# Performance work log

Hardware: AMD Instinct MI355X
Metric: run time of the kernel (lower is better)

Reference implementation:

```python
import jax, jax.numpy as jnp
import numpy as np

D_MODEL = 1024


def setup_inputs() -> dict:
    key = jax.random.key(0)
    ks = jax.random.split(key, 7)
    s = 1.0 / np.sqrt(D_MODEL)
    return {
        "x": jax.random.normal(ks[0], (4, 4096, D_MODEL), dtype=jnp.float32),
        "Wq": jax.random.normal(ks[1], (D_MODEL, D_MODEL), dtype=jnp.float32) * s,
        "bq": jax.random.normal(ks[2], (D_MODEL,), dtype=jnp.float32) * s,
        "Wk": jax.random.normal(ks[3], (D_MODEL, D_MODEL), dtype=jnp.float32) * s,
        "bk": jax.random.normal(ks[4], (D_MODEL,), dtype=jnp.float32) * s,
        "Wv": jax.random.normal(ks[5], (D_MODEL, D_MODEL), dtype=jnp.float32) * s,
        "bv": jax.random.normal(ks[6], (D_MODEL,), dtype=jnp.float32) * s,
    }


def reference(x, Wq, bq, Wk, bk, Wv, bv):
    # nn.Linear: y = x @ W.T + b
    Q = jnp.einsum("bsd,ed->bse", x, Wq) + bq  # [B,S,D]
    K = jnp.einsum("bsd,ed->bse", x, Wk) + bk
    V = jnp.einsum("bsd,ed->bse", x, Wv) + bv
    scale = 1.0 / jnp.sqrt(jnp.asarray(x.shape[-1], dtype=x.dtype))
    KV = jnp.einsum("bsd,bse->bde", K, V) * scale  # [B,D,D]
    E = jnp.einsum("bsd,bde->bse", Q, KV)  # [B,S,D]
    return E
```

## Files before the change

### kernel.cpp

```cpp
#include <hip/hip_runtime.h>
#include <hip/hip_fp16.h>


#define BATCH 4
#define SEQ   4096
#define DM    1024

typedef _Float16 h8 __attribute__((ext_vector_type(8)));
typedef _Float16 h4 __attribute__((ext_vector_type(4)));
typedef float    f4 __attribute__((ext_vector_type(4)));

__device__ inline void gload_lds16(const _Float16* g, _Float16* l) {
    __builtin_amdgcn_global_load_lds(
        (const __attribute__((address_space(1))) void*)g,
        (__attribute__((address_space(3))) void*)l,
        16, 0, 0);
}

__device__ inline int xcd_swz(int bid, int grid) {
    const int q = grid >> 3;
    return (bid & 7) * q + (bid >> 3);
}

__device__ inline float doth(const _Float16* wr, const float* v, int lane) {
    float s = 0.f;
    #pragma unroll
    for (int i = 0; i < 2; ++i) {
        const int k = i * 512 + lane * 8;
        h8 wv = *(const h8*)&wr[k];
        f4 v0 = *(const f4*)&v[k];
        f4 v1 = *(const f4*)&v[k + 4];
        s += (float)wv[0] * v0.x + (float)wv[1] * v0.y +
             (float)wv[2] * v0.z + (float)wv[3] * v0.w +
             (float)wv[4] * v1.x + (float)wv[5] * v1.y +
             (float)wv[6] * v1.z + (float)wv[7] * v1.w;
    }
    return s;
}
__device__ inline float dotf(const float* a, const float* b, int lane) {
    float s = 0.f;
    #pragma unroll
    for (int i = 0; i < 4; ++i) {
        const int k = i * 256 + lane * 4;
        f4 x = *(const f4*)&a[k];
        f4 y = *(const f4*)&b[k];
        s += x.x * y.x + x.y * y.y + x.z * y.z + x.w * y.w;
    }
    return s;
}
__device__ inline float wred(float s) {
    #pragma unroll
    for (int off = 32; off; off >>= 1) s += __shfl_down(s, off);
    return s;
}

__global__ __launch_bounds__(256) void cvt_x(
    const float* __restrict__ src, _Float16* __restrict__ dstT,
    _Float16* __restrict__ dstRM, int R, int C)
{
    __shared__ float tile[64][65];
    const long zoff = (long)blockIdx.z * R * C;
    src += zoff; dstT += zoff; dstRM += zoff;
    const int r0 = blockIdx.y * 64;
    const int c0 = blockIdx.x * 64;
    const int t  = threadIdx.x;
    const int tr = t >> 4;
    const int tc = (t & 15) * 4;
    #pragma unroll
    for (int i = 0; i < 4; ++i) {
        const int r = tr + i * 16;
        f4 v = *(const f4*)&src[(long)(r0 + r) * C + c0 + tc];
        tile[r][tc + 0] = v.x; tile[r][tc + 1] = v.y;
        tile[r][tc + 2] = v.z; tile[r][tc + 3] = v.w;
        h4 h = { (_Float16)v.x, (_Float16)v.y, (_Float16)v.z, (_Float16)v.w };
        *(h4*)&dstRM[(long)(r0 + r) * C + c0 + tc] = h;
    }
    __syncthreads();
    #pragma unroll
    for (int i = 0; i < 4; ++i) {
        const int c = tr + i * 16;
        h4 h = { (_Float16)tile[tc + 0][c], (_Float16)tile[tc + 1][c],
                 (_Float16)tile[tc + 2][c], (_Float16)tile[tc + 3][c] };
        *(h4*)&dstT[(long)(c0 + c) * R + r0 + tc] = h;
    }
}

__global__ __launch_bounds__(256) void wcvt(
    const float* __restrict__ Wq, const float* __restrict__ Wk,
    const float* __restrict__ Wv,
    _Float16* __restrict__ Wqt, _Float16* __restrict__ Wkt,
    _Float16* __restrict__ Wkh, _Float16* __restrict__ Wvh)
{
    __shared__ float tile[64][65];
    const int z = blockIdx.z;
    const float* src = z == 0 ? Wq : (z == 1 ? Wk : Wv);
    _Float16* dstT  = z == 0 ? Wqt : (z == 1 ? Wkt : nullptr);
    _Float16* dstRM = z == 0 ? nullptr : (z == 1 ? Wkh : Wvh);
    const int r0 = blockIdx.y * 64;
    const int c0 = blockIdx.x * 64;
    const int t  = threadIdx.x;
    const int tr = t >> 4;
    const int tc = (t & 15) * 4;
    #pragma unroll
    for (int i = 0; i < 4; ++i) {
        const int r = tr + i * 16;
        f4 v = *(const f4*)&src[(long)(r0 + r) * DM + c0 + tc];
        tile[r][tc + 0] = v.x; tile[r][tc + 1] = v.y;
        tile[r][tc + 2] = v.z; tile[r][tc + 3] = v.w;
        if (dstRM) {
            h4 h = { (_Float16)v.x, (_Float16)v.y, (_Float16)v.z, (_Float16)v.w };
            *(h4*)&dstRM[(long)(r0 + r) * DM + c0 + tc] = h;
        }
    }
    __syncthreads();
    if (dstT) {
        #pragma unroll
        for (int i = 0; i < 4; ++i) {
            const int c = tr + i * 16;
            h4 h = { (_Float16)tile[tc + 0][c], (_Float16)tile[tc + 1][c],
                     (_Float16)tile[tc + 2][c], (_Float16)tile[tc + 3][c] };
            *(h4*)&dstT[(long)(c0 + c) * DM + r0 + tc] = h;
        }
    }
}

__global__ __launch_bounds__(256) void rowsum_xt(
    const _Float16* __restrict__ xt, float* __restrict__ xs)
{
    const int gw   = blockIdx.x * 4 + (threadIdx.x >> 6);
    const int lane = threadIdx.x & 63;
    const _Float16* row = xt + (long)gw * SEQ;
    float s = 0.f;
    #pragma unroll
    for (int i = 0; i < SEQ; i += 512) {
        h8 v = *(const h8*)&row[i + lane * 8];
        #pragma unroll
        for (int j = 0; j < 8; ++j) s += (float)v[j];
    }
    s = wred(s);
    if (lane == 0) xs[gw] = s;
}

__global__ __launch_bounds__(256) void gemv_misc(
    const _Float16* __restrict__ Wvh, const _Float16* __restrict__ Wkh,
    const _Float16* __restrict__ Wqt, const _Float16* __restrict__ Wkt,
    const float* __restrict__ xs, const float* __restrict__ bv,
    const float* __restrict__ bk, const float* __restrict__ bq,
    float* __restrict__ vecs)
{
    const int gw   = blockIdx.x * 4 + (threadIdx.x >> 6);
    const int lane = threadIdx.x & 63;
    const _Float16* wr;
    const float* v;
    if (gw < 4096)      { wr = Wvh + (long)(gw & 1023) * DM; v = xs + (gw >> 10) * DM; }
    else if (gw < 8192) { wr = Wkh + (long)(gw & 1023) * DM; v = xs + ((gw - 4096) >> 10) * DM; }
    else if (gw < 9216) { wr = Wqt + (long)(gw - 8192) * DM; v = bk; }
    else                { wr = Wkt + (long)(gw - 9216) * DM; v = bq; }
    float s = wred(doth(wr, v, lane));
    if (lane == 0) {
        if (gw < 4096) s += (float)SEQ * bv[gw & 1023];
        vecs[gw] = s;
    }
}

__global__ __launch_bounds__(256) void gemv_qw(
    const _Float16* __restrict__ Wqt, const float* __restrict__ w,
    const float* __restrict__ bq, const float* __restrict__ bk,
    float* __restrict__ qw, float* __restrict__ sv)
{
    const int gw   = blockIdx.x * 4 + (threadIdx.x >> 6);
    const int lane = threadIdx.x & 63;
    if (gw < 4096) {
        float s = wred(doth(Wqt + (long)(gw & 1023) * DM, w + (gw >> 10) * DM, lane));
        if (lane == 0) qw[gw] = s;
    } else if (gw == 4096) {
        float s = wred(dotf(bq, bk, lane));
        if (lane == 0) sv[0] = s;
    } else if (gw <= 4100) {
        float s = wred(dotf(bq, w + (gw - 4097) * DM, lane));
        if (lane == 0) sv[1 + (gw - 4097)] = s;
    }
}

__global__ __launch_bounds__(256) void gemv_cv(
    const _Float16* __restrict__ Ph, const float* __restrict__ kb,
    const float* __restrict__ u2, const float* __restrict__ bv,
    const float* __restrict__ sv, float* __restrict__ cv)
{
    const int gw   = blockIdx.x * 4 + (threadIdx.x >> 6);
    const int lane = threadIdx.x & 63;
    const int b    = gw >> 10;
    const int e    = gw & 1023;
    float s = wred(doth(Ph + (long)b * DM * DM + (long)e * DM, kb, lane));
    if (lane == 0)
        cv[gw] = s + (sv[0] * u2[gw] + sv[1 + b] * bv[e]) * 0.03125f;
}

__global__ __launch_bounds__(256) void reduce_gh(
    const _Float16* __restrict__ parts, _Float16* __restrict__ Gh)
{
    const long DD_ = (long)DM * DM;
    const long i = ((long)blockIdx.x * 256 + threadIdx.x) * 8;
    const long b = i >> 20;
    const long r = i & (DD_ - 1);
    const _Float16* p = parts + b * 4 * DD_ + r;
    h8 v0 = *(const h8*)&p[0];
    h8 v1 = *(const h8*)&p[DD_];
    h8 v2 = *(const h8*)&p[2 * DD_];
    h8 v3 = *(const h8*)&p[3 * DD_];
    h8 o;
    #pragma unroll
    for (int j = 0; j < 8; ++j) {
        float s = (float)v0[j] + (float)v1[j] + (float)v2[j] + (float)v3[j];
        o[j] = (_Float16)(s * 0.03125f);
    }
    *(h8*)&Gh[i] = o;
}

template<typename OutT, int BIAS>
__global__ __launch_bounds__(512, 1) void gemm8p(
    const _Float16* __restrict__ A, const _Float16* __restrict__ B,
    OutT* __restrict__ C,
    int K, int lda, int ldb, int ldc, int tilesX, int perZ,
    long aZ, long bZ, long cZ, int sk, long aK, long bK,
    const float* __restrict__ bc1, long bc1Z, float alpha)
{
    __shared__ _Float16 lds[2 * 32768];

    const int L  = xcd_swz(blockIdx.x, gridDim.x);
    const int z  = L / perZ;
    const int r0 = L - z * perZ;
    const int zb = z / sk;
    const int zk = z - zb * sk;
    A += (long)zb * aZ + (long)zk * aK;
    B += (long)zb * bZ + (long)zk * bK;
    C += (long)z * cZ;
    const float* pc1 = (BIAS == 1) ? bc1 + (long)zb * bc1Z : nullptr;

    const int tileM = (r0 / tilesX) * 256;
    const int tileN = (r0 % tilesX) * 256;
    const int tid   = threadIdx.x;
    const int lane  = tid & 63;
    const int wave  = tid >> 6;
    const int wr    = wave >> 2;
    const int wc    = wave & 3;
    const int la    = lane & 15;
    const int kg    = lane >> 4;

    auto stageA = [&](int buf, int mq, int kt) {
        _Float16* dst = &lds[buf * 32768 + mq * 8192];
        const int k0 = kt * 64;
        #pragma unroll
        for (int i = 0; i < 2; ++i) {
            const int U = i * 512 + tid;
            const int R = U >> 3, s = U & 7;
            const int gr = tileM + (R >> 6) * 128 + mq * 64 + (R & 63);
            gload_lds16(&A[(long)gr * lda + k0 + ((s ^ (R & 7)) << 3)], dst + U * 8);
        }
    };
    auto stageB = [&](int buf, int nq, int kt) {
        _Float16* dst = &lds[buf * 32768 + 16384 + nq * 8192];
        const int k0 = kt * 64;
        #pragma unroll
        for (int i = 0; i < 2; ++i) {
            const int U = i * 512 + tid;
            const int R = U >> 3, s = U & 7;
            const int gn = tileN + (R >> 5) * 64 + nq * 32 + (R & 31);
            gload_lds16(&B[(long)gn * ldb + k0 + ((s ^ (R & 7)) << 3)], dst + U * 8);
        }
    };

    f4 acc[8][4] = {};
    h8 af[4][2];
    h8 bf[2][2][2];

    auto readA = [&](int buf, int mq) {
        const _Float16* Ab = &lds[buf * 32768 + mq * 8192];
        #pragma unroll
        for (int mi = 0; mi < 4; ++mi)
            #pragma unroll
            for (int kk = 0; kk < 2; ++kk) {
                const int R = wr * 64 + mi * 16 + la;
                const int s = kk * 4 + kg;
                af[mi][kk] = *(const h8*)&Ab[R * 64 + ((s ^ (R & 7)) << 3)];
            }
    };
    auto readB = [&](int buf, int nq) {
        const _Float16* Bb = &lds[buf * 32768 + 16384 + nq * 8192];
        #pragma unroll
        for (int ni = 0; ni < 2; ++ni)
            #pragma unroll
            for (int kk = 0; kk < 2; ++kk) {
                const int R = wc * 32 + ni * 16 + la;
                const int s = kk * 4 + kg;
                bf[nq][ni][kk] = *(const h8*)&Bb[R * 64 + ((s ^ (R & 7)) << 3)];
            }
    };
    auto mfmaQ = [&](int mq, int nq) {
        __builtin_amdgcn_s_setprio(1);
        #pragma unroll
        for (int mi = 0; mi < 4; ++mi)
            #pragma unroll
            for (int ni = 0; ni < 2; ++ni)
                #pragma unroll
                for (int kk = 0; kk < 2; ++kk)
                    acc[mq * 4 + mi][nq * 2 + ni] =
                        __builtin_amdgcn_mfma_f32_16x16x32_f16(
                            af[mi][kk], bf[nq][ni][kk],
                            acc[mq * 4 + mi][nq * 2 + ni], 0, 0, 0);
        __builtin_amdgcn_s_setprio(0);
    };

    const int NT = K >> 6;

    stageA(0, 0, 0); stageA(0, 1, 0); stageB(0, 0, 0); stageB(0, 1, 0);
    if (NT > 1) {
        stageA(1, 0, 1); stageB(1, 0, 1);
        asm volatile("s_waitcnt vmcnt(4)" ::: "memory");
    } else {
        asm volatile("s_waitcnt vmcnt(0)" ::: "memory");
    }
    __builtin_amdgcn_sched_barrier(0);
    __builtin_amdgcn_s_barrier();

    for (int j = 0; j < NT; ++j) {
        const int buf = j & 1;
        readA(buf, 0); readB(buf, 0);
        if (j + 1 < NT) stageA(buf ^ 1, 1, j + 1);
        asm volatile("s_waitcnt lgkmcnt(8)" ::: "memory");
        __builtin_amdgcn_s_barrier();
        asm volatile("s_waitcnt lgkmcnt(0)" ::: "memory");
        __builtin_amdgcn_sched_barrier(0);
        mfmaQ(0, 0);
        __builtin_amdgcn_s_barrier();
        readB(buf, 1);
        if (j + 1 < NT) stageB(buf ^ 1, 1, j + 1);
        __builtin_amdgcn_s_barrier();
        asm volatile("s_waitcnt lgkmcnt(0)" ::: "memory");
        __builtin_amdgcn_sched_barrier(0);
        mfmaQ(0, 1);
        __builtin_amdgcn_s_barrier();
        readA(buf, 1);
        if (j + 2 < NT) stageA(buf, 0, j + 2);
        __builtin_amdgcn_s_barrier();
        asm volatile("s_waitcnt lgkmcnt(0)" ::: "memory");
        __builtin_amdgcn_sched_barrier(0);
        mfmaQ(1, 0);
        __builtin_amdgcn_s_barrier();
        if (j + 2 < NT) stageB(buf, 0, j + 2);
        __builtin_amdgcn_s_barrier();
        mfmaQ(1, 1);
        if (j + 2 < NT) {
            asm volatile("s_waitcnt vmcnt(4)" ::: "memory");
        } else if (j + 1 < NT) {
            asm volatile("s_waitcnt vmcnt(0)" ::: "memory");
        }
        __builtin_amdgcn_sched_barrier(0);
        __builtin_amdgcn_s_barrier();
    }

    #pragma unroll
    for (int mf = 0; mf < 8; ++mf) {
        #pragma unroll
        for (int nf = 0; nf < 4; ++nf) {
            const int col = tileN + wc * 64 + nf * 16 + la;
            #pragma unroll
            for (int jj = 0; jj < 4; ++jj) {
                const int row = tileM + wr * 128 + mf * 16 + kg * 4 + jj;
                float v = acc[mf][nf][jj] * alpha;
                if (BIAS == 1) v += pc1[col];
                C[(long)row * ldc + col] = (OutT)v;
            }
        }
    }
}

template<int BIAS>
__global__ __launch_bounds__(256) void gemm64(
    const _Float16* __restrict__ A, const _Float16* __restrict__ B,
    _Float16* __restrict__ C,
    const _Float16* __restrict__ A2, const _Float16* __restrict__ B2,
    _Float16* __restrict__ C2, int zSplit,
    int K, int lda, int ldb, int ldc, int tilesX, int perZ,
    long aZ, long bZ, long cZ,
    const float* __restrict__ bc1, long bc1Z,
    const float* __restrict__ br1, long br1Z,
    const float* __restrict__ bc2, long bc2Z,
    const float* __restrict__ br2, long br2Z,
    float alpha, float beta)
{
    __shared__ _Float16 As[64 * 64];
    __shared__ _Float16 Bs[64 * 64];

    const int L  = xcd_swz(blockIdx.x, gridDim.x);
    int z        = L / perZ;
    const int r0 = L - z * perZ;
    if (z >= zSplit) { A = A2; B = B2; C = C2; z = 0; }
    A += (long)z * aZ;
    B += (long)z * bZ;
    C += (long)z * cZ;
    const float* pc1 = nullptr; const float* pr1 = nullptr;
    const float* pc2 = nullptr; const float* pr2 = nullptr;
    if (BIAS == 3) {
        pc1 = bc1 + (long)z * bc1Z; pr1 = br1 + (long)z * br1Z;
        pc2 = bc2 + (long)z * bc2Z; pr2 = br2 + (long)z * br2Z;
    }

    const int tileM = (r0 / tilesX) * 64;
    const int tileN = (r0 % tilesX) * 64;
    const int tid   = threadIdx.x;
    const int lane  = tid & 63;
    const int wave  = tid >> 6;
    const int wm    = (wave >> 1) * 32;
    const int wn    = (wave & 1) * 32;
    const int srow  = tid >> 3;
    const int sslot = tid & 7;

    f4 acc[2][2] = {};
    const int arow = lane & 15;
    const int kg   = lane >> 4;

    for (int k0 = 0; k0 < K; k0 += 64) {
        #pragma unroll
        for (int i = 0; i < 2; ++i) {
            const int row   = i * 32 + srow;
            const int gslot = sslot ^ (row & 7);
            gload_lds16(&A[(long)(tileM + row) * lda + k0 + gslot * 8],
                        &As[row * 64 + sslot * 8]);
            gload_lds16(&B[(long)(tileN + row) * ldb + k0 + gslot * 8],
                        &Bs[row * 64 + sslot * 8]);
        }
        __syncthreads();

        #pragma unroll
        for (int kk = 0; kk < 64; kk += 32) {
            h8 af[2], bf[2];
            #pragma unroll
            for (int m = 0; m < 2; ++m) {
                const int rr   = wm + m * 16 + arow;
                const int slot = (kk >> 3) + kg;
                af[m] = *(const h8*)&As[rr * 64 + ((slot ^ (rr & 7)) << 3)];
            }
            #pragma unroll
            for (int n = 0; n < 2; ++n) {
                const int rr   = wn + n * 16 + arow;
                const int slot = (kk >> 3) + kg;
                bf[n] = *(const h8*)&Bs[rr * 64 + ((slot ^ (rr & 7)) << 3)];
            }
            #pragma unroll
            for (int m = 0; m < 2; ++m)
                #pragma unroll
                for (int n = 0; n < 2; ++n)
                    acc[m][n] = __builtin_amdgcn_mfma_f32_16x16x32_f16(
                        af[m], bf[n], acc[m][n], 0, 0, 0);
        }
        __syncthreads();
    }

    #pragma unroll
    for (int m = 0; m < 2; ++m) {
        #pragma unroll
        for (int n = 0; n < 2; ++n) {
            const int col = tileN + wn + n * 16 + arow;
            #pragma unroll
            for (int j = 0; j < 4; ++j) {
                const int row = tileM + wm + m * 16 + (lane >> 4) * 4 + j;
                float v = acc[m][n][j] * alpha;
                if (BIAS == 3) v += beta * (pc1[col] * pr1[row] + pc2[col] * pr2[row]);
                C[(long)row * ldc + col] = (_Float16)v;
            }
        }
    }
}

extern "C" void kernel_launch(void* const* d_in, const int* in_sizes, int n_in,
                              void* d_out, int out_size, void* d_ws, size_t ws_size,
                              hipStream_t stream)
{
    const float* x  = (const float*)d_in[0];
    const float* Wq = (const float*)d_in[1];
    const float* bq = (const float*)d_in[2];
    const float* Wk = (const float*)d_in[3];
    const float* bk = (const float*)d_in[4];
    const float* Wv = (const float*)d_in[5];
    const float* bv = (const float*)d_in[6];
    float* out = (float*)d_out;

    const long DD = (long)DM * DM;
    const long DS = (long)DM * SEQ;
    const long MB = 1024l * 1024;

    char* base = (char*)d_ws;
    _Float16* xh   = (_Float16*)base;
    _Float16* xt   = (_Float16*)(base + 32 * MB);
    _Float16* Gh   = xt;
    _Float16* Ph   = (_Float16*)(base + 40 * MB);
    _Float16* Rth  = (_Float16*)(base + 48 * MB);
    _Float16* Wqt  = (_Float16*)(base + 64 * MB);
    _Float16* Wkh  = (_Float16*)(base + 66 * MB);
    _Float16* Wvh  = (_Float16*)(base + 68 * MB);
    _Float16* Wkt  = (_Float16*)(base + 70 * MB);
    _Float16* Mh   = (_Float16*)(base + 72 * MB);
    float*    vecs = (float*)(base + 74 * MB);
    float*    u2   = vecs;
    float*    w    = vecs + 4096;
    float*    qk   = vecs + 8192;
    float*    kb   = vecs + 9216;
    float*    xs   = vecs + 10240;
    float*    qw   = vecs + 14336;
    float*    cv   = vecs + 18432;
    float*    sv   = vecs + 22528;
    _Float16* parts = (_Float16*)d_out;

    cvt_x<<<dim3(16, 64, 4), 256, 0, stream>>>(x, xt, xh, SEQ, DM);
    wcvt<<<dim3(16, 16, 3), 256, 0, stream>>>(Wq, Wk, Wv, Wqt, Wkt, Wkh, Wvh);

    rowsum_xt<<<1024, 256, 0, stream>>>(xt, xs);

    gemv_misc<<<2560, 256, 0, stream>>>(Wvh, Wkh, Wqt, Wkt, xs, bv, bk, bq, vecs);

    gemv_qw<<<1026, 256, 0, stream>>>(Wqt, w, bq, bk, qw, sv);

    gemm8p<_Float16, 0><<<256, 512, 0, stream>>>(
        xt, xt, parts, 1024, SEQ, SEQ, DM, 4, 16,
        DS, DS, DD, 4, 1024, 1024, nullptr, 0, 1.0f);

    reduce_gh<<<2048, 256, 0, stream>>>(parts, Gh);

    gemm64<0><<<1280, 256, 0, stream>>>(
        Wvh, Gh, Ph, Wqt, Wkt, Mh, 4,
        1024, DM, DM, DM, 16, 256,
        0, DD, DD,
        nullptr, 0, nullptr, 0, nullptr, 0, nullptr, 0, 1.0f, 0.f);

    gemv_cv<<<1024, 256, 0, stream>>>(Ph, kb, u2, bv, sv, cv);

    gemm64<3><<<1024, 256, 0, stream>>>(
        Ph, Mh, Rth, nullptr, nullptr, nullptr, 99,
        1024, DM, DM, DM, 16, 256,
        DD, 0, DD,
        qk, 0, u2, 1024, qw, 1024, bv, 0, 1.0f, 0.03125f);

    gemm8p<float, 1><<<256, 512, 0, stream>>>(
        xh, Rth, out, 1024, DM, DM, DM, 4, 64,
        DS, DD, DS, 1, 0, 0, cv, 1024, 1.0f);
}
```

Baseline: 168.1 us.

## Exploit symmetry of Gram matrix with triangular split-K tiles and fuse rowsum

The x^T x Gram product is now computed only for the 10 upper-triangular 256x256 tiles per batch. Each tile is split into 6 K-chunks of uneven length so 240 blocks cover the work, and a new reduce kernel sums the partials and mirrors off-diagonal tiles via an LDS transpose. The separate column-sum kernel is removed; cvt_x now accumulates the sums with atomicAdd after a memset. This cuts redundant MFMA work and one kernel launch, at the cost of fp32 atomics and a more complex reduce.

```diff
diff --git a/kernel.cpp b/kernel.cpp
--- a/kernel.cpp
+++ b/kernel.cpp
@@ -56,9 +56,10 @@
 
 __global__ __launch_bounds__(256) void cvt_x(
     const float* __restrict__ src, _Float16* __restrict__ dstT,
-    _Float16* __restrict__ dstRM, int R, int C)
+    _Float16* __restrict__ dstRM, float* __restrict__ xs, int R, int C)
 {
     __shared__ float tile[64][65];
+    __shared__ float red[4][64];
     const long zoff = (long)blockIdx.z * R * C;
     src += zoff; dstT += zoff; dstRM += zoff;
     const int r0 = blockIdx.y * 64;
@@ -83,6 +84,18 @@
                  (_Float16)tile[tc + 2][c], (_Float16)tile[tc + 3][c] };
         *(h4*)&dstT[(long)(c0 + c) * R + r0 + tc] = h;
     }
+    {
+        const int cc = t & 63;
+        const int rb = (t >> 6) * 16;
+        float ps = 0.f;
+        #pragma unroll
+        for (int r = 0; r < 16; ++r) ps += tile[rb + r][cc];
+        red[t >> 6][cc] = ps;
+    }
+    __syncthreads();
+    if (t < 64)
+        atomicAdd(&xs[blockIdx.z * DM + c0 + t],
+                  red[0][t] + red[1][t] + red[2][t] + red[3][t]);
 }
 
 __global__ __launch_bounds__(256) void wcvt(
@@ -122,23 +135,6 @@
             *(h4*)&dstT[(long)(c0 + c) * DM + r0 + tc] = h;
         }
     }
-}
-
-__global__ __launch_bounds__(256) void rowsum_xt(
-    const _Float16* __restrict__ xt, float* __restrict__ xs)
-{
-    const int gw   = blockIdx.x * 4 + (threadIdx.x >> 6);
-    const int lane = threadIdx.x & 63;
-    const _Float16* row = xt + (long)gw * SEQ;
-    float s = 0.f;
-    #pragma unroll
-    for (int i = 0; i < SEQ; i += 512) {
-        h8 v = *(const h8*)&row[i + lane * 8];
-        #pragma unroll
-        for (int j = 0; j < 8; ++j) s += (float)v[j];
-    }
-    s = wred(s);
-    if (lane == 0) xs[gw] = s;
 }
 
 __global__ __launch_bounds__(256) void gemv_misc(
@@ -196,28 +192,54 @@
         cv[gw] = s + (sv[0] * u2[gw] + sv[1 + b] * bv[e]) * 0.03125f;
 }
 
-__global__ __launch_bounds__(256) void reduce_gh(
+__global__ __launch_bounds__(256) void reduce_tri(
     const _Float16* __restrict__ parts, _Float16* __restrict__ Gh)
 {
+    __shared__ _Float16 lds[64][72];
+    const int bid = blockIdx.x;
+    const int job = bid >> 4;
+    const int ch  = bid & 15;
+    const int b   = job / 10;
+    const int p   = job - b * 10;
+    const int ti  = p >= 6 ? 3 : (p >= 3 ? 2 : (p >= 1 ? 1 : 0));
+    const int tj  = p - ((ti * (ti + 1)) >> 1);
+    const int li  = (ch >> 2) * 64;
+    const int lj  = (ch & 3) * 64;
+    const int t   = threadIdx.x;
+    const int c8  = (t & 7) * 8;
     const long DD_ = (long)DM * DM;
-    const long i = ((long)blockIdx.x * 256 + threadIdx.x) * 8;
-    const long b = i >> 20;
-    const long r = i & (DD_ - 1);
-    const _Float16* p = parts + b * 4 * DD_ + r;
-    h8 v0 = *(const h8*)&p[0];
-    h8 v1 = *(const h8*)&p[DD_];
-    h8 v2 = *(const h8*)&p[2 * DD_];
-    h8 v3 = *(const h8*)&p[3 * DD_];
-    h8 o;
-    #pragma unroll
-    for (int j = 0; j < 8; ++j) {
-        float s = (float)v0[j] + (float)v1[j] + (float)v2[j] + (float)v3[j];
-        o[j] = (_Float16)(s * 0.03125f);
-    }
-    *(h8*)&Gh[i] = o;
-}
-
-template<typename OutT, int BIAS>
+
+    h8 o[2];
+    #pragma unroll
+    for (int h = 0; h < 2; ++h) {
+        const int r = (t >> 3) + h * 32;
+        float a[8] = {};
+        #pragma unroll
+        for (int s = 0; s < 6; ++s) {
+            const _Float16* src = parts + ((long)(job * 6 + s) << 16);
+            h8 v = *(const h8*)&src[(li + r) * 256 + lj + c8];
+            #pragma unroll
+            for (int j = 0; j < 8; ++j) a[j] += (float)v[j];
+        }
+        #pragma unroll
+        for (int j = 0; j < 8; ++j) o[h][j] = (_Float16)(a[j] * 0.03125f);
+        *(h8*)&Gh[b * DD_ + (long)(ti * 256 + li + r) * DM + tj * 256 + lj + c8] = o[h];
+        *(h8*)&lds[r][c8] = o[h];
+    }
+    if (ti != tj) {
+        __syncthreads();
+        #pragma unroll
+        for (int h = 0; h < 2; ++h) {
+            const int r = (t >> 3) + h * 32;
+            h8 m;
+            #pragma unroll
+            for (int j = 0; j < 8; ++j) m[j] = lds[c8 + j][r];
+            *(h8*)&Gh[b * DD_ + (long)(tj * 256 + lj + r) * DM + ti * 256 + li + c8] = m;
+        }
+    }
+}
+
+template<typename OutT, int BIAS, int TRI>
 __global__ __launch_bounds__(512, 1) void gemm8p(
     const _Float16* __restrict__ A, const _Float16* __restrict__ B,
     OutT* __restrict__ C,
@@ -227,25 +249,45 @@
 {
     __shared__ _Float16 lds[2 * 32768];
 
-    const int L  = xcd_swz(blockIdx.x, gridDim.x);
-    const int z  = L / perZ;
-    const int r0 = L - z * perZ;
-    const int zb = z / sk;
-    const int zk = z - zb * sk;
-    A += (long)zb * aZ + (long)zk * aK;
-    B += (long)zb * bZ + (long)zk * bK;
-    C += (long)z * cZ;
-    const float* pc1 = (BIAS == 1) ? bc1 + (long)zb * bc1Z : nullptr;
-
-    const int tileM = (r0 / tilesX) * 256;
-    const int tileN = (r0 % tilesX) * 256;
-    const int tid   = threadIdx.x;
-    const int lane  = tid & 63;
-    const int wave  = tid >> 6;
-    const int wr    = wave >> 2;
-    const int wc    = wave & 3;
-    const int la    = lane & 15;
-    const int kg    = lane >> 4;
+    const int L = xcd_swz(blockIdx.x, gridDim.x);
+    int tileM, tileN, cTileM, cTileN, NT;
+    const float* pc1 = nullptr;
+    if (TRI) {
+        const int job = L / 6;
+        const int s   = L - job * 6;
+        const int b   = job / 10;
+        const int p   = job - b * 10;
+        const int ti  = p >= 6 ? 3 : (p >= 3 ? 2 : (p >= 1 ? 1 : 0));
+        const int tj  = p - ((ti * (ti + 1)) >> 1);
+        const int kOff = s < 4 ? s * 704 : 2816 + (s - 4) * 640;
+        NT = s < 4 ? 11 : 10;
+        A += (long)b * aZ + kOff;
+        B += (long)b * aZ + kOff;
+        C += (long)(job * 6 + s) * cZ;
+        tileM = ti * 256; tileN = tj * 256;
+        cTileM = 0; cTileN = 0;
+    } else {
+        const int z  = L / perZ;
+        const int r0 = L - z * perZ;
+        const int zb = z / sk;
+        const int zk = z - zb * sk;
+        A += (long)zb * aZ + (long)zk * aK;
+        B += (long)zb * bZ + (long)zk * bK;
+        C += (long)z * cZ;
+        if (BIAS == 1) pc1 = bc1 + (long)zb * bc1Z;
+        tileM = (r0 / tilesX) * 256;
+        tileN = (r0 % tilesX) * 256;
+        cTileM = tileM; cTileN = tileN;
+        NT = K >> 6;
+    }
+
+    const int tid  = threadIdx.x;
+    const int lane = tid & 63;
+    const int wave = tid >> 6;
+    const int wr   = wave >> 2;
+    const int wc   = wave & 3;
+    const int la   = lane & 15;
+    const int kg   = lane >> 4;
 
     auto stageA = [&](int buf, int mq, int kt) {
         _Float16* dst = &lds[buf * 32768 + mq * 8192];
@@ -311,8 +353,6 @@
         __builtin_amdgcn_s_setprio(0);
     };
 
-    const int NT = K >> 6;
-
     stageA(0, 0, 0); stageA(0, 1, 0); stageB(0, 0, 0); stageB(0, 1, 0);
     if (NT > 1) {
         stageA(1, 0, 1); stageB(1, 0, 1);
@@ -363,10 +403,10 @@
     for (int mf = 0; mf < 8; ++mf) {
         #pragma unroll
         for (int nf = 0; nf < 4; ++nf) {
-            const int col = tileN + wc * 64 + nf * 16 + la;
+            const int col = cTileN + wc * 64 + nf * 16 + la;
             #pragma unroll
             for (int jj = 0; jj < 4; ++jj) {
-                const int row = tileM + wr * 128 + mf * 16 + kg * 4 + jj;
+                const int row = cTileM + wr * 128 + mf * 16 + kg * 4 + jj;
                 float v = acc[mf][nf][jj] * alpha;
                 if (BIAS == 1) v += pc1[col];
                 C[(long)row * ldc + col] = (OutT)v;
@@ -512,20 +552,20 @@
     float*    sv   = vecs + 22528;
     _Float16* parts = (_Float16*)d_out;
 
-    cvt_x<<<dim3(16, 64, 4), 256, 0, stream>>>(x, xt, xh, SEQ, DM);
+    hipMemsetAsync(xs, 0, BATCH * DM * sizeof(float), stream);
+
+    cvt_x<<<dim3(16, 64, 4), 256, 0, stream>>>(x, xt, xh, xs, SEQ, DM);
     wcvt<<<dim3(16, 16, 3), 256, 0, stream>>>(Wq, Wk, Wv, Wqt, Wkt, Wkh, Wvh);
 
-    rowsum_xt<<<1024, 256, 0, stream>>>(xt, xs);
-
     gemv_misc<<<2560, 256, 0, stream>>>(Wvh, Wkh, Wqt, Wkt, xs, bv, bk, bq, vecs);
 
     gemv_qw<<<1026, 256, 0, stream>>>(Wqt, w, bq, bk, qw, sv);
 
-    gemm8p<_Float16, 0><<<256, 512, 0, stream>>>(
-        xt, xt, parts, 1024, SEQ, SEQ, DM, 4, 16,
-        DS, DS, DD, 4, 1024, 1024, nullptr, 0, 1.0f);
-
-    reduce_gh<<<2048, 256, 0, stream>>>(parts, Gh);
+    gemm8p<_Float16, 0, 1><<<240, 512, 0, stream>>>(
+        xt, xt, parts, 4096, SEQ, SEQ, 256, 0, 0,
+        DS, DS, 65536, 1, 0, 0, nullptr, 0, 1.0f);
+
+    reduce_tri<<<640, 256, 0, stream>>>(parts, Gh);
 
     gemm64<0><<<1280, 256, 0, stream>>>(
         Wvh, Gh, Ph, Wqt, Wkt, Mh, 4,
@@ -541,7 +581,7 @@
         DD, 0, DD,
         qk, 0, u2, 1024, qw, 1024, bv, 0, 1.0f, 0.03125f);
 
-    gemm8p<float, 1><<<256, 512, 0, stream>>>(
+    gemm8p<float, 1, 0><<<256, 512, 0, stream>>>(
         xh, Rth, out, 1024, DM, DM, DM, 4, 64,
         DS, DD, DS, 1, 0, 0, cv, 1024, 1.0f);
 }
```

Result: faster. 156.9 us (-6.7%).
